# Optimization experiments

Measured on AMD Instinct MI355X. Metric: run time of the kernel, lower is better.

The kernel has to match this reference:

```python
import jax, jax.numpy as jnp
import numpy as np


def setup_inputs() -> dict:
    key = jax.random.key(0)
    ks = jax.random.split(key, 11)
    B, L, D = 8, 4096, 1024
    n_head = 16
    s = D ** -0.5
    return {
        "q": jax.random.normal(ks[0], (B, L, D), jnp.float32),
        "k": jax.random.normal(ks[1], (B, L, D), jnp.float32),
        "v": jax.random.normal(ks[2], (B, L, D), jnp.float32),
        "Wq": jax.random.normal(ks[3], (D, D), jnp.float32) * s,
        "bq": jax.random.normal(ks[4], (D,), jnp.float32) * 0.01,
        "Wk": jax.random.normal(ks[5], (D, D), jnp.float32) * s,
        "bk": jax.random.normal(ks[6], (D,), jnp.float32) * 0.01,
        "Wv": jax.random.normal(ks[7], (D, D), jnp.float32) * s,
        "bv": jax.random.normal(ks[8], (D,), jnp.float32) * 0.01,
        "Wo": jax.random.normal(ks[9], (D, D), jnp.float32) * s,
        "bo": jax.random.normal(ks[10], (D,), jnp.float32) * 0.01,
        "n_head": n_head,
    }


def reference(q, k, v, Wq, bq, Wk, bk, Wv, bv, Wo, bo, n_head):
    B, L, D = q.shape
    hd = D // n_head
    scale = jnp.asarray(hd, q.dtype) ** -0.5

    # Faithful to original: view(B, n_head, L, hd).transpose(1, 2) -> (B, L, n_head, hd)
    def split(x):
        return x.reshape(B, n_head, L, hd).transpose(0, 2, 1, 3)

    Q = split(q @ Wq + bq)
    K = split(k @ Wk + bk)
    V = split(v @ Wv + bv)

    # attention over the HEAD axis, per position: (B, L, n_head, n_head)
    scores = jnp.einsum('blhd,bljd->blhj', Q, K) * scale
    weights = jax.nn.softmax(scores, axis=-1)
    ctx = jnp.einsum('blhj,bljd->blhd', weights, V)

    # transpose(1,2).contiguous().view(B, L, D)
    ctx = ctx.transpose(0, 2, 1, 3).reshape(B, L, D)
    out = ctx @ Wo + bo
    return (out, weights)
```

## Files before the change

### kernel.cpp

```cpp
#include <hip/hip_runtime.h>
#include <hip/hip_bf16.h>
#include <stdint.h>

typedef unsigned short u16;
typedef unsigned int   u32;
typedef __attribute__((ext_vector_type(8))) short bf16x8;
typedef __attribute__((ext_vector_type(4))) float f32x4;

#define GLAS  __attribute__((address_space(1)))
#define LDSAS __attribute__((address_space(3)))

__device__ __forceinline__ void gl_lds16(const void* g, void* l) {
    __builtin_amdgcn_global_load_lds((const GLAS u32*)(uintptr_t)g,
                                     (LDSAS u32*)(u32)(uintptr_t)l, 16, 0, 0);
}

__device__ __forceinline__ u16 f2bf_rne(float f) {
    u32 u = __float_as_uint(f);
    u32 r = u + 0x7fffu + ((u >> 16) & 1u);
    return (u16)(r >> 16);
}
__device__ __forceinline__ u32 pk_bf2(float a, float b) {
    __hip_bfloat162 h = __float22bfloat162_rn(float2{a, b});
    u32 u; __builtin_memcpy(&u, &h, 4);
    return u;
}
__device__ __forceinline__ float bfbits_lo(u32 p) { return __uint_as_float(p << 16); }
__device__ __forceinline__ float bfbits_hi(u32 p) { return __uint_as_float(p & 0xffff0000u); }

__device__ __forceinline__ void unpack8(uint4 u, float* f) {
    f[0] = bfbits_lo(u.x); f[1] = bfbits_hi(u.x);
    f[2] = bfbits_lo(u.y); f[3] = bfbits_hi(u.y);
    f[4] = bfbits_lo(u.z); f[5] = bfbits_hi(u.z);
    f[6] = bfbits_lo(u.w); f[7] = bfbits_hi(u.w);
}

struct WtArgs { const float* W[4]; u16* WT[4]; };

__global__ __launch_bounds__(256) void wtrans(WtArgs a) {
    const int z = blockIdx.z;
    const float* __restrict__ W = a.W[z];
    u16* __restrict__ WT = a.WT[z];
    __shared__ float tile[64][65];
    const int n0 = blockIdx.x * 64, k0 = blockIdx.y * 64;
    const int tid = threadIdx.x;
    const int r = tid >> 6, c = tid & 63;
    #pragma unroll
    for (int p = 0; p < 16; ++p) {
        const int row = p * 4 + r;
        tile[row][c] = W[(size_t)(k0 + row) * 1024 + n0 + c];
    }
    __syncthreads();
    #pragma unroll
    for (int p = 0; p < 16; ++p) {
        const int row = p * 4 + r;
        WT[(size_t)(n0 + row) * 1024 + k0 + c] = f2bf_rne(tile[c][row]);
    }
}

struct CvtArgs { const float* src[3]; u16* dst[3]; };

__global__ __launch_bounds__(256) void cvt3(CvtArgs a, int n8) {
    const int z = blockIdx.y;
    const float* __restrict__ src = a.src[z];
    u16* __restrict__ dst = a.dst[z];
    const int stride = gridDim.x * 256;
    for (int i = blockIdx.x * 256 + threadIdx.x; i < n8; i += stride) {
        const float4* s = (const float4*)(src + (size_t)i * 8);
        float4 x = s[0], y = s[1];
        uint4 o;
        o.x = pk_bf2(x.x, x.y); o.y = pk_bf2(x.z, x.w);
        o.z = pk_bf2(y.x, y.y); o.w = pk_bf2(y.z, y.w);
        *(uint4*)(dst + (size_t)i * 8) = o;
    }
}

struct GemmArgs { const u16* A[3]; const u16* BT[3]; const float* bias[3]; void* C[3]; };

template<bool OUT_F32>
__global__ __launch_bounds__(256, 2)
void gemm_bt(GemmArgs ga, int M, int N, int K) {
    __shared__ u16 As[128 * 32];
    __shared__ u16 Bs[128 * 32];
    const int L = blockIdx.x;
    const int z = L >> 11;
    const int r = L & 2047;
    const int xcd = r & 7;
    const int slot = r >> 3;
    const int m0 = (xcd * 32 + (slot >> 3)) * 128;
    const int n0 = (slot & 7) * 128;

    const u16*   __restrict__ A    = ga.A[z];
    const u16*   __restrict__ BT   = ga.BT[z];
    const float* __restrict__ bias = ga.bias[z];
    const int tid = threadIdx.x;
    const int lane = tid & 63;
    const int wave = tid >> 6;

    f32x4 acc[4][4] = {};

    const int srow = lane >> 2;
    const int scol = (lane & 3) * 8;

    for (int k0 = 0; k0 < K; k0 += 32) {
        #pragma unroll
        for (int cc = 0; cc < 2; ++cc) {
            const int chunk = cc * 4 + wave;
            gl_lds16(A  + (size_t)(m0 + chunk * 16 + srow) * K + (k0 + scol),
                     &As[chunk * 512]);
            gl_lds16(BT + (size_t)(n0 + chunk * 16 + srow) * K + (k0 + scol),
                     &Bs[chunk * 512]);
        }
        __syncthreads();

        const int wm = (wave >> 1) * 64;
        const int wn = (wave & 1) * 64;
        const int fr = lane & 15;
        const int fk = (lane >> 4) * 8;
        bf16x8 af[4], bfr[4];
        #pragma unroll
        for (int i = 0; i < 4; ++i) af[i]  = *(const bf16x8*)&As[(wm + i * 16 + fr) * 32 + fk];
        #pragma unroll
        for (int j = 0; j < 4; ++j) bfr[j] = *(const bf16x8*)&Bs[(wn + j * 16 + fr) * 32 + fk];
        #pragma unroll
        for (int i = 0; i < 4; ++i)
            #pragma unroll
            for (int j = 0; j < 4; ++j)
                acc[i][j] = __builtin_amdgcn_mfma_f32_16x16x32_bf16(af[i], bfr[j], acc[i][j], 0, 0, 0);
        __syncthreads();
    }

    const int wm = (wave >> 1) * 64;
    const int wn = (wave & 1) * 64;
    const int r0 = m0 + wm + (lane >> 4) * 4;
    const int c0 = n0 + wn + (lane & 15);
    #pragma unroll
    for (int j = 0; j < 4; ++j) {
        const int col = c0 + j * 16;
        const float bv = bias[col];
        #pragma unroll
        for (int i = 0; i < 4; ++i) {
            #pragma unroll
            for (int rr = 0; rr < 4; ++rr) {
                const int row = r0 + i * 16 + rr;
                const float v = acc[i][j][rr] + bv;
                if constexpr (OUT_F32) ((float*)ga.C[z])[(size_t)row * N + col] = v;
                else                   ((u16*)ga.C[z])[(size_t)row * N + col] = f2bf_rne(v);
            }
        }
    }
    (void)M;
}

__global__ __launch_bounds__(256, 2)
void attn(const u16* __restrict__ QL, const u16* __restrict__ KL, const u16* __restrict__ VL,
          u16* __restrict__ CTX, float* __restrict__ WOUT) {
    __shared__ u16 Ks[16 * 1024];
    __shared__ u16 Vs[16 * 1024];
    const int bg = blockIdx.x;
    const int b = bg >> 8, g = bg & 255;
    const int tid = threadIdx.x, lane = tid & 63, wave = tid >> 6;
    const size_t boff = (size_t)b * (4096 * 1024);

    for (int it = 0; it < 8; ++it) {
        const int c = it * 4 + wave;
        const int row = c >> 1, half = c & 1;
        const size_t gidx = boff + (size_t)(row * 256 + g) * 1024 + half * 512 + lane * 8;
        gl_lds16(KL + gidx, &Ks[c * 512]);
        gl_lds16(VL + gidx, &Vs[c * 512]);
    }
    __syncthreads();

    const int t = tid >> 4, h = tid & 15;
    float qf[64];
    const u16* qp = QL + boff + (size_t)(h * 256 + g) * 1024 + t * 64;
    #pragma unroll
    for (int c8 = 0; c8 < 8; ++c8) {
        uint4 u = *(const uint4*)(qp + c8 * 8);
        unpack8(u, &qf[c8 * 8]);
    }
    float s[16];
    #pragma unroll 1
    for (int j = 0; j < 16; ++j) {
        const u16* kp = &Ks[j * 1024 + t * 64];
        float a = 0.f;
        #pragma unroll
        for (int c8 = 0; c8 < 8; ++c8) {
            uint4 u = *(const uint4*)(kp + c8 * 8);
            float kf[8]; unpack8(u, kf);
            #pragma unroll
            for (int d = 0; d < 8; ++d) a = fmaf(qf[c8 * 8 + d], kf[d], a);
        }
        s[j] = a * 0.125f;
    }
    float mx = s[0];
    #pragma unroll
    for (int j = 1; j < 16; ++j) mx = fmaxf(mx, s[j]);
    float w[16], sum = 0.f;
    #pragma unroll
    for (int j = 0; j < 16; ++j) { w[j] = __expf(s[j] - mx); sum += w[j]; }
    const float inv = 1.f / sum;
    #pragma unroll
    for (int j = 0; j < 16; ++j) w[j] *= inv;
    {
        float4* wp = (float4*)(WOUT + ((size_t)((b * 4096 + g * 16 + t) * 16 + h) * 16));
        wp[0] = float4{w[0],  w[1],  w[2],  w[3]};
        wp[1] = float4{w[4],  w[5],  w[6],  w[7]};
        wp[2] = float4{w[8],  w[9],  w[10], w[11]};
        wp[3] = float4{w[12], w[13], w[14], w[15]};
    }
    float cx[64];
    #pragma unroll
    for (int d = 0; d < 64; ++d) cx[d] = 0.f;
    #pragma unroll 1
    for (int j = 0; j < 16; ++j) {
        const u16* vp = &Vs[j * 1024 + t * 64];
        const float wj = w[j];
        #pragma unroll
        for (int c8 = 0; c8 < 8; ++c8) {
            uint4 u = *(const uint4*)(vp + c8 * 8);
            float vf[8]; unpack8(u, vf);
            #pragma unroll
            for (int d = 0; d < 8; ++d) cx[c8 * 8 + d] = fmaf(wj, vf[d], cx[c8 * 8 + d]);
        }
    }
    u16* cp = CTX + boff + (size_t)(h * 256 + g) * 1024 + t * 64;
    #pragma unroll
    for (int c8 = 0; c8 < 8; ++c8) {
        uint4 o;
        o.x = pk_bf2(cx[c8 * 8 + 0], cx[c8 * 8 + 1]);
        o.y = pk_bf2(cx[c8 * 8 + 2], cx[c8 * 8 + 3]);
        o.z = pk_bf2(cx[c8 * 8 + 4], cx[c8 * 8 + 5]);
        o.w = pk_bf2(cx[c8 * 8 + 6], cx[c8 * 8 + 7]);
        *(uint4*)(cp + c8 * 8) = o;
    }
}

extern "C" void kernel_launch(void* const* d_in, const int* in_sizes, int n_in,
                              void* d_out, int out_size, void* d_ws, size_t ws_size,
                              hipStream_t stream) {
    const float* q  = (const float*)d_in[0];
    const float* k  = (const float*)d_in[1];
    const float* v  = (const float*)d_in[2];
    const float* Wq = (const float*)d_in[3];
    const float* bq = (const float*)d_in[4];
    const float* Wk = (const float*)d_in[5];
    const float* bk = (const float*)d_in[6];
    const float* Wv = (const float*)d_in[7];
    const float* bv = (const float*)d_in[8];
    const float* Wo = (const float*)d_in[9];
    const float* bo = (const float*)d_in[10];

    const int M = 32768, D = 1024;
    const size_t MD = (size_t)M * D;
    const int n8 = (int)(MD / 8);

    u16* WT0 = (u16*)d_ws;
    u16* WT1 = WT0 + 1048576;
    u16* WT2 = WT1 + 1048576;
    u16* WT3 = WT2 + 1048576;
    u16* big0 = WT3 + 1048576;

    float* out  = (float*)d_out;
    float* wout = out + MD;

    WtArgs wa{{Wq, Wk, Wv, Wo}, {WT0, WT1, WT2, WT3}};
    wtrans<<<dim3(16, 16, 4), 256, 0, stream>>>(wa);

    const size_t needBig = 2ull * (4ull * 1048576 + 6ull * MD);
    if (ws_size >= needBig) {
        u16* QB = big0;      u16* KB = QB + MD;  u16* VB = KB + MD;
        u16* QL = VB + MD;   u16* KL = QL + MD;  u16* VL = KL + MD;
        u16* CTX = QB;
        CvtArgs ca{{q, k, v}, {QB, KB, VB}};
        cvt3<<<dim3(1024, 3), 256, 0, stream>>>(ca, n8);
        GemmArgs g1{{QB, KB, VB}, {WT0, WT1, WT2}, {bq, bk, bv}, {QL, KL, VL}};
        gemm_bt<false><<<dim3(3 * 2048), 256, 0, stream>>>(g1, M, D, D);
        attn<<<dim3(2048), 256, 0, stream>>>(QL, KL, VL, CTX, wout);
        GemmArgs g2{{CTX, CTX, CTX}, {WT3, WT3, WT3}, {bo, bo, bo}, {out, out, out}};
        gemm_bt<true><<<dim3(2048), 256, 0, stream>>>(g2, M, D, D);
    } else {
        u16* AB = big0;
        u16* QL = AB + MD;   u16* KL = QL + MD;  u16* VL = KL + MD;
        u16* CTX = AB;
        const float* src[3]  = {q, k, v};
        const float* bia[3]  = {bq, bk, bv};
        u16* wt[3]           = {WT0, WT1, WT2};
        u16* dst[3]          = {QL, KL, VL};
        for (int i = 0; i < 3; ++i) {
            CvtArgs ca{{src[i], src[i], src[i]}, {AB, AB, AB}};
            cvt3<<<dim3(1024, 1), 256, 0, stream>>>(ca, n8);
            GemmArgs g1{{AB, AB, AB}, {wt[i], wt[i], wt[i]}, {bia[i], bia[i], bia[i]},
                        {dst[i], dst[i], dst[i]}};
            gemm_bt<false><<<dim3(2048), 256, 0, stream>>>(g1, M, D, D);
        }
        attn<<<dim3(2048), 256, 0, stream>>>(QL, KL, VL, CTX, wout);
        GemmArgs g2{{CTX, CTX, CTX}, {WT3, WT3, WT3}, {bo, bo, bo}, {out, out, out}};
        gemm_bt<true><<<dim3(2048), 256, 0, stream>>>(g2, M, D, D);
    }
}
```

Baseline: 905.8 us.

## Deepen GEMM K-tile with XOR swizzle, split attention head dims across threads

The GEMM now stages 64-wide K slices instead of 32 and applies an XOR swizzle to LDS columns. This halves the number of barriers per tile and is meant to reduce LDS bank conflicts on fragment reads. The attention kernel uses 512 threads, each handling half of a head's 64 dims and combining partial dot products with a cross-lane shuffle. It also reuses a single LDS buffer for K and then V, which halves LDS use and per-thread registers to allow more resident waves. The cvt kernel launches twice as many blocks. The trade-off is an extra barrier and serialized K/V loads in attention.

New measurement: 860.7 us. -5.0%, faster.

```diff
diff --git a/kernel.cpp b/kernel.cpp
--- a/kernel.cpp
+++ b/kernel.cpp
@@ -80,8 +80,8 @@
 template<bool OUT_F32>
 __global__ __launch_bounds__(256, 2)
 void gemm_bt(GemmArgs ga, int M, int N, int K) {
-    __shared__ u16 As[128 * 32];
-    __shared__ u16 Bs[128 * 32];
+    __shared__ u16 As[128 * 64];
+    __shared__ u16 Bs[128 * 64];
     const int L = blockIdx.x;
     const int z = L >> 11;
     const int r = L & 2047;
@@ -99,39 +99,50 @@
 
     f32x4 acc[4][4] = {};
 
-    const int srow = lane >> 2;
-    const int scol = (lane & 3) * 8;
-
-    for (int k0 = 0; k0 < K; k0 += 32) {
-        #pragma unroll
-        for (int cc = 0; cc < 2; ++cc) {
-            const int chunk = cc * 4 + wave;
-            gl_lds16(A  + (size_t)(m0 + chunk * 16 + srow) * K + (k0 + scol),
-                     &As[chunk * 512]);
-            gl_lds16(BT + (size_t)(n0 + chunk * 16 + srow) * K + (k0 + scol),
-                     &Bs[chunk * 512]);
-        }
-        __syncthreads();
-
-        const int wm = (wave >> 1) * 64;
-        const int wn = (wave & 1) * 64;
-        const int fr = lane & 15;
-        const int fk = (lane >> 4) * 8;
-        bf16x8 af[4], bfr[4];
-        #pragma unroll
-        for (int i = 0; i < 4; ++i) af[i]  = *(const bf16x8*)&As[(wm + i * 16 + fr) * 32 + fk];
-        #pragma unroll
-        for (int j = 0; j < 4; ++j) bfr[j] = *(const bf16x8*)&Bs[(wn + j * 16 + fr) * 32 + fk];
-        #pragma unroll
-        for (int i = 0; i < 4; ++i)
-            #pragma unroll
-            for (int j = 0; j < 4; ++j)
-                acc[i][j] = __builtin_amdgcn_mfma_f32_16x16x32_bf16(af[i], bfr[j], acc[i][j], 0, 0, 0);
-        __syncthreads();
-    }
+    const int srow = lane >> 3;
+    const int scol = ((lane & 7) ^ srow) * 8;
 
     const int wm = (wave >> 1) * 64;
     const int wn = (wave & 1) * 64;
+    const int fr = lane & 15;
+    const int fk = (lane >> 4) * 8;
+    const int fx = (fr & 7) << 3;
+
+    for (int k0 = 0; k0 < K; k0 += 64) {
+        #pragma unroll
+        for (int cc = 0; cc < 4; ++cc) {
+            const int chunk = cc * 4 + wave;
+            gl_lds16(A  + (size_t)(m0 + chunk * 8 + srow) * K + (k0 + scol),
+                     &As[chunk * 512]);
+            gl_lds16(BT + (size_t)(n0 + chunk * 8 + srow) * K + (k0 + scol),
+                     &Bs[chunk * 512]);
+        }
+        __syncthreads();
+
+        bf16x8 af[4][2], bfr[4][2];
+        #pragma unroll
+        for (int i = 0; i < 4; ++i) {
+            const int rowb = (wm + i * 16 + fr) * 64;
+            af[i][0] = *(const bf16x8*)&As[rowb + ((0 * 32 + fk) ^ fx)];
+            af[i][1] = *(const bf16x8*)&As[rowb + ((1 * 32 + fk) ^ fx)];
+        }
+        #pragma unroll
+        for (int j = 0; j < 4; ++j) {
+            const int rowb = (wn + j * 16 + fr) * 64;
+            bfr[j][0] = *(const bf16x8*)&Bs[rowb + ((0 * 32 + fk) ^ fx)];
+            bfr[j][1] = *(const bf16x8*)&Bs[rowb + ((1 * 32 + fk) ^ fx)];
+        }
+        #pragma unroll
+        for (int kk = 0; kk < 2; ++kk)
+            #pragma unroll
+            for (int i = 0; i < 4; ++i)
+                #pragma unroll
+                for (int j = 0; j < 4; ++j)
+                    acc[i][j] = __builtin_amdgcn_mfma_f32_16x16x32_bf16(
+                        af[i][kk], bfr[j][kk], acc[i][j], 0, 0, 0);
+        __syncthreads();
+    }
+
     const int r0 = m0 + wm + (lane >> 4) * 4;
     const int c0 = n0 + wn + (lane & 15);
     #pragma unroll
@@ -152,87 +163,102 @@
     (void)M;
 }
 
-__global__ __launch_bounds__(256, 2)
+__global__ __launch_bounds__(512, 4)
 void attn(const u16* __restrict__ QL, const u16* __restrict__ KL, const u16* __restrict__ VL,
           u16* __restrict__ CTX, float* __restrict__ WOUT) {
-    __shared__ u16 Ks[16 * 1024];
-    __shared__ u16 Vs[16 * 1024];
+    __shared__ u16 KVs[16 * 1024];
     const int bg = blockIdx.x;
     const int b = bg >> 8, g = bg & 255;
     const int tid = threadIdx.x, lane = tid & 63, wave = tid >> 6;
     const size_t boff = (size_t)b * (4096 * 1024);
 
-    for (int it = 0; it < 8; ++it) {
-        const int c = it * 4 + wave;
+    #pragma unroll
+    for (int it = 0; it < 4; ++it) {
+        const int c = it * 8 + wave;
         const int row = c >> 1, half = c & 1;
         const size_t gidx = boff + (size_t)(row * 256 + g) * 1024 + half * 512 + lane * 8;
-        gl_lds16(KL + gidx, &Ks[c * 512]);
-        gl_lds16(VL + gidx, &Vs[c * 512]);
+        gl_lds16(KL + gidx, &KVs[c * 512]);
+    }
+
+    const int h = tid & 15, dh = (tid >> 4) & 1, t = tid >> 5;
+    const int dof = t * 64 + dh * 32;
+
+    float qf[32];
+    const u16* qp = QL + boff + (size_t)(h * 256 + g) * 1024 + dof;
+    #pragma unroll
+    for (int c4 = 0; c4 < 4; ++c4) {
+        uint4 u = *(const uint4*)(qp + c4 * 8);
+        unpack8(u, &qf[c4 * 8]);
     }
     __syncthreads();
 
-    const int t = tid >> 4, h = tid & 15;
-    float qf[64];
-    const u16* qp = QL + boff + (size_t)(h * 256 + g) * 1024 + t * 64;
-    #pragma unroll
-    for (int c8 = 0; c8 < 8; ++c8) {
-        uint4 u = *(const uint4*)(qp + c8 * 8);
-        unpack8(u, &qf[c8 * 8]);
-    }
-    float s[16];
+    float w[16];
     #pragma unroll 1
     for (int j = 0; j < 16; ++j) {
-        const u16* kp = &Ks[j * 1024 + t * 64];
+        const u16* kp = &KVs[j * 1024 + dof];
         float a = 0.f;
         #pragma unroll
-        for (int c8 = 0; c8 < 8; ++c8) {
-            uint4 u = *(const uint4*)(kp + c8 * 8);
+        for (int c4 = 0; c4 < 4; ++c4) {
+            uint4 u = *(const uint4*)(kp + c4 * 8);
             float kf[8]; unpack8(u, kf);
             #pragma unroll
-            for (int d = 0; d < 8; ++d) a = fmaf(qf[c8 * 8 + d], kf[d], a);
-        }
-        s[j] = a * 0.125f;
-    }
-    float mx = s[0];
-    #pragma unroll
-    for (int j = 1; j < 16; ++j) mx = fmaxf(mx, s[j]);
-    float w[16], sum = 0.f;
-    #pragma unroll
-    for (int j = 0; j < 16; ++j) { w[j] = __expf(s[j] - mx); sum += w[j]; }
+            for (int d = 0; d < 8; ++d) a = fmaf(qf[c4 * 8 + d], kf[d], a);
+        }
+        a += __shfl_xor(a, 16);
+        w[j] = a * 0.125f;
+    }
+    float mx = w[0];
+    #pragma unroll
+    for (int j = 1; j < 16; ++j) mx = fmaxf(mx, w[j]);
+    float sum = 0.f;
+    #pragma unroll
+    for (int j = 0; j < 16; ++j) { w[j] = __expf(w[j] - mx); sum += w[j]; }
     const float inv = 1.f / sum;
     #pragma unroll
     for (int j = 0; j < 16; ++j) w[j] *= inv;
-    {
+
+    __syncthreads();
+
+    #pragma unroll
+    for (int it = 0; it < 4; ++it) {
+        const int c = it * 8 + wave;
+        const int row = c >> 1, half = c & 1;
+        const size_t gidx = boff + (size_t)(row * 256 + g) * 1024 + half * 512 + lane * 8;
+        gl_lds16(VL + gidx, &KVs[c * 512]);
+    }
+    __syncthreads();
+
+    float cx[32];
+    #pragma unroll
+    for (int d = 0; d < 32; ++d) cx[d] = 0.f;
+    #pragma unroll 1
+    for (int j = 0; j < 16; ++j) {
+        const u16* vp = &KVs[j * 1024 + dof];
+        const float wj = w[j];
+        #pragma unroll
+        for (int c4 = 0; c4 < 4; ++c4) {
+            uint4 u = *(const uint4*)(vp + c4 * 8);
+            float vf[8]; unpack8(u, vf);
+            #pragma unroll
+            for (int d = 0; d < 8; ++d) cx[c4 * 8 + d] = fmaf(wj, vf[d], cx[c4 * 8 + d]);
+        }
+    }
+    u16* cp = CTX + boff + (size_t)(h * 256 + g) * 1024 + dof;
+    #pragma unroll
+    for (int c4 = 0; c4 < 4; ++c4) {
+        uint4 o;
+        o.x = pk_bf2(cx[c4 * 8 + 0], cx[c4 * 8 + 1]);
+        o.y = pk_bf2(cx[c4 * 8 + 2], cx[c4 * 8 + 3]);
+        o.z = pk_bf2(cx[c4 * 8 + 4], cx[c4 * 8 + 5]);
+        o.w = pk_bf2(cx[c4 * 8 + 6], cx[c4 * 8 + 7]);
+        *(uint4*)(cp + c4 * 8) = o;
+    }
+    if (dh == 0) {
         float4* wp = (float4*)(WOUT + ((size_t)((b * 4096 + g * 16 + t) * 16 + h) * 16));
         wp[0] = float4{w[0],  w[1],  w[2],  w[3]};
         wp[1] = float4{w[4],  w[5],  w[6],  w[7]};
         wp[2] = float4{w[8],  w[9],  w[10], w[11]};
         wp[3] = float4{w[12], w[13], w[14], w[15]};
-    }
-    float cx[64];
-    #pragma unroll
-    for (int d = 0; d < 64; ++d) cx[d] = 0.f;
-    #pragma unroll 1
-    for (int j = 0; j < 16; ++j) {
-        const u16* vp = &Vs[j * 1024 + t * 64];
-        const float wj = w[j];
-        #pragma unroll
-        for (int c8 = 0; c8 < 8; ++c8) {
-            uint4 u = *(const uint4*)(vp + c8 * 8);
-            float vf[8]; unpack8(u, vf);
-            #pragma unroll
-            for (int d = 0; d < 8; ++d) cx[c8 * 8 + d] = fmaf(wj, vf[d], cx[c8 * 8 + d]);
-        }
-    }
-    u16* cp = CTX + boff + (size_t)(h * 256 + g) * 1024 + t * 64;
-    #pragma unroll
-    for (int c8 = 0; c8 < 8; ++c8) {
-        uint4 o;
-        o.x = pk_bf2(cx[c8 * 8 + 0], cx[c8 * 8 + 1]);
-        o.y = pk_bf2(cx[c8 * 8 + 2], cx[c8 * 8 + 3]);
-        o.z = pk_bf2(cx[c8 * 8 + 4], cx[c8 * 8 + 5]);
-        o.w = pk_bf2(cx[c8 * 8 + 6], cx[c8 * 8 + 7]);
-        *(uint4*)(cp + c8 * 8) = o;
     }
 }
 
@@ -273,10 +299,10 @@
         u16* QL = VB + MD;   u16* KL = QL + MD;  u16* VL = KL + MD;
         u16* CTX = QB;
         CvtArgs ca{{q, k, v}, {QB, KB, VB}};
-        cvt3<<<dim3(1024, 3), 256, 0, stream>>>(ca, n8);
+        cvt3<<<dim3(2048, 3), 256, 0, stream>>>(ca, n8);
         GemmArgs g1{{QB, KB, VB}, {WT0, WT1, WT2}, {bq, bk, bv}, {QL, KL, VL}};
         gemm_bt<false><<<dim3(3 * 2048), 256, 0, stream>>>(g1, M, D, D);
-        attn<<<dim3(2048), 256, 0, stream>>>(QL, KL, VL, CTX, wout);
+        attn<<<dim3(2048), 512, 0, stream>>>(QL, KL, VL, CTX, wout);
         GemmArgs g2{{CTX, CTX, CTX}, {WT3, WT3, WT3}, {bo, bo, bo}, {out, out, out}};
         gemm_bt<true><<<dim3(2048), 256, 0, stream>>>(g2, M, D, D);
     } else {
@@ -289,12 +315,12 @@
         u16* dst[3]          = {QL, KL, VL};
         for (int i = 0; i < 3; ++i) {
             CvtArgs ca{{src[i], src[i], src[i]}, {AB, AB, AB}};
-            cvt3<<<dim3(1024, 1), 256, 0, stream>>>(ca, n8);
+            cvt3<<<dim3(2048, 1), 256, 0, stream>>>(ca, n8);
             GemmArgs g1{{AB, AB, AB}, {wt[i], wt[i], wt[i]}, {bia[i], bia[i], bia[i]},
                         {dst[i], dst[i], dst[i]}};
             gemm_bt<false><<<dim3(2048), 256, 0, stream>>>(g1, M, D, D);
         }
-        attn<<<dim3(2048), 256, 0, stream>>>(QL, KL, VL, CTX, wout);
+        attn<<<dim3(2048), 512, 0, stream>>>(QL, KL, VL, CTX, wout);
         GemmArgs g2{{CTX, CTX, CTX}, {WT3, WT3, WT3}, {bo, bo, bo}, {out, out, out}};
         gemm_bt<true><<<dim3(2048), 256, 0, stream>>>(g2, M, D, D);
     }
```
